# Kernel optimization log

Hardware: AMD Instinct MI355X
Metric: run time of the kernel (lower is better)

## Reference

```python
import math
import jax, jax.numpy as jnp
import numpy as np

N, E = 4096, 131072
IN_DIM, HID_DIM, OUT_DIM = 1024, 512, 128
PE_IN, PE_HID, K = 128, 64, 10
PE_ALPHA, PE_BETA = 0.1, 0.5


def _glorot(k, shape):
    fan = shape[0] + shape[-1]
    return jax.random.normal(k, shape, dtype=jnp.float32) * (2.0 / fan) ** 0.5


def setup_inputs() -> dict:
    key = jax.random.key(0)
    ks = jax.random.split(key, 12)
    return {
        "node_feat": jax.random.normal(ks[0], (N, IN_DIM), dtype=jnp.float32),
        "edge_index": jax.random.randint(ks[1], (2, E), 0, N, dtype=jnp.int64),
        "pos_enc": jax.random.normal(ks[2], (N, PE_IN), dtype=jnp.float32),
        "lin1_w": _glorot(ks[3], (IN_DIM, HID_DIM)),
        "lin1_b": jnp.zeros((HID_DIM,), jnp.float32),
        "lin2_w": _glorot(ks[4], (HID_DIM, OUT_DIM)),
        "lin2_b": jnp.zeros((OUT_DIM,), jnp.float32),
        "pe_w": _glorot(ks[5], (PE_IN, PE_HID)),
        "pe_b": jnp.zeros((PE_HID,), jnp.float32),
        "cor_w": _glorot(ks[6], (PE_HID, PE_HID)),
        "cor_b": jnp.zeros((PE_HID,), jnp.float32),
        "gate_w": _glorot(ks[7], (K + 1, PE_HID)),
        "gate_b": jnp.zeros((K + 1,), jnp.float32),
        "temp": jnp.ones((K + 1,), jnp.float32),
    }


def reference(node_feat, edge_index, pos_enc, lin1_w, lin1_b, lin2_w, lin2_b,
              pe_w, pe_b, cor_w, cor_b, gate_w, gate_b, temp):
    n = node_feat.shape[0]
    src, dst = edge_index[0], edge_index[1]
    ew = jnp.ones(src.shape[0], dtype=node_feat.dtype)

    # sym-normalized adjacency A_norm = D^-1/2 A D^-1/2 (deg on source row, per PyG get_laplacian)
    deg = jax.ops.segment_sum(ew, src, num_segments=n)
    dinv = jnp.where(deg > 0, deg ** -0.5, 0.0)
    wl = dinv[src] * dinv[dst]

    def anorm(x):  # scatter-add message passing: out[i] = sum_j w_ij x[j]
        return jax.ops.segment_sum(wl[:, None] * x[src], dst, num_segments=n)

    # gcn_norm with self-loops: Ahat = Dhat^-1/2 (A + I) Dhat^-1/2 (deg on target col)
    deg2 = jax.ops.segment_sum(ew, dst, num_segments=n) + 1.0
    d2 = deg2 ** -0.5
    wg = d2[src] * d2[dst]

    def ahat(p):
        return jax.ops.segment_sum(wg[:, None] * p[src], dst, num_segments=n) + (d2 * d2)[:, None] * p

    # encoders
    pe = jnp.tanh(pos_enc @ pe_w + pe_b)
    x = jax.nn.relu(node_feat @ lin1_w + lin1_b) @ lin2_w + lin2_b

    TEMP = jax.nn.relu(temp)
    # tmp[k] = (2I - L)^k x, and (2I - L)x = x + A_norm x
    tmp = [x]
    for _ in range(K):
        x = x + anorm(x)
        tmp.append(x)

    coeff = [math.comb(K, i) / 2 ** K for i in range(K + 1)]
    gamma0 = TEMP[0] * jax.nn.sigmoid((pe @ gate_w[0])[:, None] + gate_b[0])  # [N,1]
    out = coeff[0] * gamma0 * tmp[K]

    raw_pe = pe
    for i in range(K):
        xi = tmp[K - i - 1]
        for _ in range(i + 1):  # apply L = I - A_norm, (i+1) times
            xi = xi - anorm(xi)
        # PE correlation propagation: dense NxN sigmoid adjacency
        c = pe @ cor_w + cor_b
        pe_corr = jax.nn.sigmoid(c @ c.T) @ pe
        pe_tpo = ahat(pe)
        pe = (1.0 + PE_BETA) * pe_tpo - PE_BETA * pe_corr
        pe = PE_ALPHA * raw_pe + (1.0 - PE_ALPHA) * pe
        pe = jnp.tanh(pe)
        gamma = TEMP[i + 1] * jax.nn.sigmoid((pe @ gate_w[i + 1])[:, None] + gate_b[i + 1])
        out = out + coeff[i + 1] * gamma * xi
    return (out, pe)
```

## Files before the change

### kernel.cpp

```cpp
#include <hip/hip_runtime.h>
#include <math.h>

constexpr int N_NODES = 4096;
constexpr int E_EDGES = 131072;
constexpr int IND     = 1024;
constexpr int HID     = 512;
constexpr int OUTD    = 128;
constexpr int PEH     = 64;
constexpr int KHOP    = 10;
constexpr int NPE     = N_NODES * PEH;
constexpr int NM      = N_NODES * OUTD;
constexpr int NCHUNK  = 16;

__constant__ float d_coeff[11] = {
    1.f/1024.f, 10.f/1024.f, 45.f/1024.f, 120.f/1024.f, 210.f/1024.f,
    252.f/1024.f, 210.f/1024.f, 120.f/1024.f, 45.f/1024.f, 10.f/1024.f, 1.f/1024.f};

__constant__ float d_beta[11][11] = {
    {1,  10, 45, 120, 210, 252, 210, 120, 45, 10, 1},
    {1,   8, 27,  48,  42,   0, -42, -48, -27, -8, -1},
    {1,   6, 13,   8, -14, -28, -14,   8,  13,  6,  1},
    {1,   4,  3,  -8, -14,   0,  14,   8,  -3, -4, -1},
    {1,   2, -3,  -8,   2,  12,   2,  -8,  -3,  2,  1},
    {1,   0, -5,   0,  10,   0, -10,   0,   5,  0, -1},
    {1,  -2, -3,   8,   2, -12,   2,   8,  -3, -2,  1},
    {1,  -4,  3,   8, -14,   0,  14,  -8,  -3,  4, -1},
    {1,  -6, 13,  -8, -14,  28, -14,  -8,  13, -6,  1},
    {1,  -8, 27, -48,  42,   0, -42,  48, -27,  8, -1},
    {1, -10, 45, -120, 210, -252, 210, -120, 45, -10, 1}};

typedef __attribute__((ext_vector_type(8))) short bf16x8;
typedef __attribute__((ext_vector_type(4))) float f32x4;

__device__ __forceinline__ void split_bf16(float x, short& h, short& l) {
    unsigned bx = __float_as_uint(x);
    h = (short)(bx >> 16);
    float hf = __uint_as_float(bx & 0xffff0000u);
    l = (short)(__float_as_uint(x - hf) >> 16);
}

__device__ __forceinline__ size_t fidx(int g, int T, int t, int h, int lane) {
    return ((((size_t)g * T + t) * 2 + h) * 64 + lane) * 8;
}

__device__ __forceinline__ int swz(int row, int col) {
    return row * 64 + (col ^ ((row & 7) << 3));
}

__global__ void k_degrees(const int* __restrict__ src, const int* __restrict__ dst,
                          int* outdeg, int* indeg) {
    int e = blockIdx.x * blockDim.x + threadIdx.x;
    if (e < E_EDGES) {
        atomicAdd(&outdeg[src[e]], 1);
        atomicAdd(&indeg[dst[e]], 1);
    }
}

__global__ void k_invs(const int* __restrict__ outdeg, const int* __restrict__ indeg,
                       float* dinv, float* d2) {
    int i = blockIdx.x * blockDim.x + threadIdx.x;
    if (i < N_NODES) {
        int od = outdeg[i];
        dinv[i] = od > 0 ? 1.0f / sqrtf((float)od) : 0.0f;
        d2[i]   = 1.0f / sqrtf((float)indeg[i] + 1.0f);
    }
}

__global__ void k_scan(const int* __restrict__ cnt, int* __restrict__ rp) {
    int lane = threadIdx.x;
    int base = lane * 64;
    int sum = 0;
    for (int j = 0; j < 64; ++j) sum += cnt[base + j];
    int incl = sum;
    for (int off = 1; off < 64; off <<= 1) {
        int nv = __shfl_up(incl, off);
        if (lane >= off) incl += nv;
    }
    int run = incl - sum;
    for (int j = 0; j < 64; ++j) { rp[base + j] = run; run += cnt[base + j]; }
    if (lane == 63) rp[N_NODES] = run;
}

__global__ void k_scatter(const int* __restrict__ src, const int* __restrict__ dst,
                          const int* __restrict__ rp, int* __restrict__ fill,
                          const float* __restrict__ dinv, const float* __restrict__ d2,
                          int* __restrict__ col, float* __restrict__ wl,
                          float* __restrict__ wg) {
    int e = blockIdx.x * blockDim.x + threadIdx.x;
    if (e < E_EDGES) {
        int s = src[e], d = dst[e];
        int pos = rp[d] + atomicAdd(&fill[d], 1);
        col[pos] = s;
        wl[pos]  = dinv[s] * dinv[d];
        wg[pos]  = d2[s] * d2[d];
    }
}

__global__ void k_split_rm(const float* __restrict__ in, ushort* __restrict__ oh,
                           ushort* __restrict__ ol, int total8) {
    int i = blockIdx.x * blockDim.x + threadIdx.x;
    if (i >= total8) return;
    int r = i >> 7, c8 = i & 127;
    float4 f0 = *(const float4*)&in[(size_t)i * 8];
    float4 f1 = *(const float4*)&in[(size_t)i * 8 + 4];
    float v[8] = {f0.x, f0.y, f0.z, f0.w, f1.x, f1.y, f1.z, f1.w};
    bf16x8 h, l;
#pragma unroll
    for (int j = 0; j < 8; ++j) {
        short hh, ll;
        split_bf16(v[j], hh, ll);
        h[j] = hh; l[j] = ll;
    }
    int t = c8 >> 3, hh2 = (c8 >> 2) & 1, lq = c8 & 3;
    size_t a = fidx(r >> 4, IND / 64, t, hh2, lq * 16 + (r & 15));
    *(bf16x8*)&oh[a] = h;
    *(bf16x8*)&ol[a] = l;
}

__global__ __launch_bounds__(256) void k_splitT(const float* __restrict__ in,
                                                ushort* __restrict__ th,
                                                ushort* __restrict__ tl,
                                                int R, int C) {
    __shared__ float tile[64][65];
    int tid = threadIdx.x;
    int r0 = blockIdx.x * 64, c0 = blockIdx.y * 64;
    int row = tid >> 2, cq = (tid & 3) * 16;
#pragma unroll
    for (int q = 0; q < 4; ++q) {
        float4 f = *(const float4*)&in[(size_t)(r0 + row) * C + c0 + cq + q * 4];
        tile[row][cq + q * 4 + 0] = f.x;
        tile[row][cq + q * 4 + 1] = f.y;
        tile[row][cq + q * 4 + 2] = f.z;
        tile[row][cq + q * 4 + 3] = f.w;
    }
    __syncthreads();
    int d = tid & 63, q = tid >> 6;
    bf16x8 h0, h1, l0, l1;
#pragma unroll
    for (int c = 0; c < 8; ++c) {
        short hh, ll;
        split_bf16(tile[q * 16 + c][d], hh, ll);
        h0[c] = hh; l0[c] = ll;
    }
#pragma unroll
    for (int c = 0; c < 8; ++c) {
        short hh, ll;
        split_bf16(tile[q * 16 + 8 + c][d], hh, ll);
        h1[c] = hh; l1[c] = ll;
    }
    int T = R / 64;
    int g = (c0 + d) >> 4, lm = (c0 + d) & 15, t = r0 >> 6, hh2 = q >> 1;
    size_t a0 = fidx(g, T, t, hh2, ((2 * q) & 3) * 16 + lm);
    size_t a1 = fidx(g, T, t, hh2, ((2 * q + 1) & 3) * 16 + lm);
    *(bf16x8*)&th[a0] = h0;
    *(bf16x8*)&th[a1] = h1;
    *(bf16x8*)&tl[a0] = l0;
    *(bf16x8*)&tl[a1] = l1;
}

template <int T, int KCH>
__global__ __launch_bounds__(256) void k_xgemm_zp(const ushort* __restrict__ apkh,
                                                  const ushort* __restrict__ apkl,
                                                  const ushort* __restrict__ bpkh,
                                                  const ushort* __restrict__ bpkl,
                                                  float* __restrict__ pout) {
    int tid = threadIdx.x;
    int w = tid >> 6, l = tid & 63;
    int ga = blockIdx.x * 4 + w;
    int gb0 = blockIdx.y * 4;
    int t0 = blockIdx.z * (KCH / 64);
    f32x4 acc[4];
#pragma unroll
    for (int n = 0; n < 4; ++n) acc[n] = (f32x4){0.f, 0.f, 0.f, 0.f};
    for (int kk = 0; kk < KCH / 64; ++kk) {
        int t = t0 + kk;
        bf16x8 Ah0 = *(const bf16x8*)&apkh[fidx(ga, T, t, 0, l)];
        bf16x8 Ah1 = *(const bf16x8*)&apkh[fidx(ga, T, t, 1, l)];
        bf16x8 Al0 = *(const bf16x8*)&apkl[fidx(ga, T, t, 0, l)];
        bf16x8 Al1 = *(const bf16x8*)&apkl[fidx(ga, T, t, 1, l)];
#pragma unroll
        for (int n = 0; n < 4; ++n) {
            bf16x8 Bh0 = *(const bf16x8*)&bpkh[fidx(gb0 + n, T, t, 0, l)];
            bf16x8 Bh1 = *(const bf16x8*)&bpkh[fidx(gb0 + n, T, t, 1, l)];
            bf16x8 Bl0 = *(const bf16x8*)&bpkl[fidx(gb0 + n, T, t, 0, l)];
            bf16x8 Bl1 = *(const bf16x8*)&bpkl[fidx(gb0 + n, T, t, 1, l)];
            acc[n] = __builtin_amdgcn_mfma_f32_16x16x32_bf16(Ah0, Bh0, acc[n], 0, 0, 0);
            acc[n] = __builtin_amdgcn_mfma_f32_16x16x32_bf16(Ah1, Bh1, acc[n], 0, 0, 0);
            acc[n] = __builtin_amdgcn_mfma_f32_16x16x32_bf16(Ah0, Bl0, acc[n], 0, 0, 0);
            acc[n] = __builtin_amdgcn_mfma_f32_16x16x32_bf16(Ah1, Bl1, acc[n], 0, 0, 0);
            acc[n] = __builtin_amdgcn_mfma_f32_16x16x32_bf16(Al0, Bh0, acc[n], 0, 0, 0);
            acc[n] = __builtin_amdgcn_mfma_f32_16x16x32_bf16(Al1, Bh1, acc[n], 0, 0, 0);
        }
    }
    size_t base = ((((size_t)blockIdx.z * gridDim.x + blockIdx.x) * gridDim.y)
                   + blockIdx.y) * 4096;
#pragma unroll
    for (int n = 0; n < 4; ++n) {
#pragma unroll
        for (int r = 0; r < 4; ++r) {
            pout[base + (size_t)(w * 16 + n * 4 + r) * 64 + l] = acc[n][r];
        }
    }
}

template <int NC, bool RELU, bool SPLIT>
__global__ void k_finzp(const float* __restrict__ pin, const float* __restrict__ bias,
                        float* __restrict__ outf, ushort* __restrict__ oh,
                        ushort* __restrict__ ol) {
    constexpr int GY = NC / 64;
    constexpr size_t ZSTEP = (size_t)64 * GY * 4096;
    int i8 = blockIdx.x * blockDim.x + threadIdx.x;
    int r = i8 / (NC / 8), c = (i8 % (NC / 8)) * 8;
    int bx = r >> 6, w = (r >> 4) & 3, lq = (r >> 2) & 3, rr = r & 3;
    int by = c >> 6, n = (c >> 4) & 3, lm0 = c & 15;
    size_t base = (((size_t)bx * GY) + by) * 4096
                  + (size_t)(w * 16 + n * 4 + rr) * 64 + lq * 16 + lm0;
    float v[8];
#pragma unroll
    for (int j = 0; j < 8; ++j) v[j] = bias[c + j];
#pragma unroll
    for (int z = 0; z < 4; ++z) {
        float4 p0 = *(const float4*)&pin[base + z * ZSTEP];
        float4 p1 = *(const float4*)&pin[base + z * ZSTEP + 4];
        v[0] += p0.x; v[1] += p0.y; v[2] += p0.z; v[3] += p0.w;
        v[4] += p1.x; v[5] += p1.y; v[6] += p1.z; v[7] += p1.w;
    }
    if (RELU) {
#pragma unroll
        for (int j = 0; j < 8; ++j) v[j] = fmaxf(v[j], 0.f);
    }
    if (SPLIT) {
        bf16x8 h, lo;
#pragma unroll
        for (int j = 0; j < 8; ++j) {
            short hh, ll;
            split_bf16(v[j], hh, ll);
            h[j] = hh; lo[j] = ll;
        }
        size_t a = fidx(r >> 4, NC / 64, c >> 6, (c >> 5) & 1,
                        ((c >> 3) & 3) * 16 + (r & 15));
        *(bf16x8*)&oh[a] = h;
        *(bf16x8*)&ol[a] = lo;
    } else {
        *(float4*)&outf[(size_t)r * NC + c] =
            make_float4(v[0], v[1], v[2], v[3]);
        *(float4*)&outf[(size_t)r * NC + c + 4] =
            make_float4(v[4], v[5], v[6], v[7]);
    }
}

__global__ __launch_bounds__(256) void k_pe0(const float* __restrict__ pos_enc,
                                             const float* __restrict__ pw,
                                             const float* __restrict__ pb,
                                             float* __restrict__ pe,
                                             float* __restrict__ raw,
                                             ushort* __restrict__ pthpk,
                                             ushort* __restrict__ ptlpk,
                                             const float* __restrict__ gw,
                                             const float* __restrict__ gb,
                                             const float* __restrict__ temp,
                                             float* __restrict__ gamma) {
    __shared__ float tile[64][65];
    int tid = threadIdx.x, w = tid >> 6, l = tid & 63;
    int nloc = w * 16 + (l >> 2);
    int nn = blockIdx.x * 64 + nloc;
    int f0 = (l & 3) * 16;
    float v[16];
#pragma unroll
    for (int f = 0; f < 16; ++f) v[f] = pb[f0 + f];
    for (int k0 = 0; k0 < 128; k0 += 4) {
        float4 pv = *(const float4*)&pos_enc[(size_t)nn * 128 + k0];
        float pa[4] = {pv.x, pv.y, pv.z, pv.w};
#pragma unroll
        for (int kk = 0; kk < 4; ++kk) {
            const float* wr = &pw[(size_t)(k0 + kk) * 64 + f0];
            float4 w0 = *(const float4*)&wr[0];
            float4 w1 = *(const float4*)&wr[4];
            float4 w2 = *(const float4*)&wr[8];
            float4 w3 = *(const float4*)&wr[12];
            float wv[16] = {w0.x, w0.y, w0.z, w0.w, w1.x, w1.y, w1.z, w1.w,
                            w2.x, w2.y, w2.z, w2.w, w3.x, w3.y, w3.z, w3.w};
#pragma unroll
            for (int f = 0; f < 16; ++f) v[f] = fmaf(pa[kk], wv[f], v[f]);
        }
    }
#pragma unroll
    for (int f = 0; f < 16; ++f) v[f] = tanhf(v[f]);
#pragma unroll
    for (int q = 0; q < 4; ++q) {
        float4 fv = make_float4(v[q * 4], v[q * 4 + 1], v[q * 4 + 2], v[q * 4 + 3]);
        *(float4*)&pe[(size_t)nn * 64 + f0 + q * 4] = fv;
        *(float4*)&raw[(size_t)nn * 64 + f0 + q * 4] = fv;
    }
    float g = 0.f;
#pragma unroll
    for (int f = 0; f < 16; ++f) g = fmaf(v[f], gw[f0 + f], g);
    g += __shfl_xor(g, 1);
    g += __shfl_xor(g, 2);
    if ((l & 3) == 0) {
        float T = temp[0];
        T = T > 0.f ? T : 0.f;
        gamma[nn] = T / (1.f + expf(-(g + gb[0])));
    }
#pragma unroll
    for (int f = 0; f < 16; ++f) tile[nloc][f0 + f] = v[f];
    __syncthreads();
    int d = l, q = w;
    bf16x8 h0, h1, l0, l1;
#pragma unroll
    for (int c = 0; c < 8; ++c) {
        short hh, ll;
        split_bf16(tile[q * 16 + c][d], hh, ll);
        h0[c] = hh; l0[c] = ll;
    }
#pragma unroll
    for (int c = 0; c < 8; ++c) {
        short hh, ll;
        split_bf16(tile[q * 16 + 8 + c][d], hh, ll);
        h1[c] = hh; l1[c] = ll;
    }
    int ng = d >> 4, lm = d & 15, tcb = blockIdx.x, hh2 = q >> 1;
    size_t a0 = fidx(ng, 64, tcb, hh2, ((2 * q) & 3) * 16 + lm);
    size_t a1 = fidx(ng, 64, tcb, hh2, ((2 * q + 1) & 3) * 16 + lm);
    *(bf16x8*)&pthpk[a0] = h0;
    *(bf16x8*)&pthpk[a1] = h1;
    *(bf16x8*)&ptlpk[a0] = l0;
    *(bf16x8*)&ptlpk[a1] = l1;
}

__global__ void k_cmat(const float* __restrict__ pe, const float* __restrict__ cw,
                       const float* __restrict__ cb, ushort* __restrict__ chpk,
                       ushort* __restrict__ clpk) {
    int t = threadIdx.x;
    int r = blockIdx.x * 4 + threadIdx.y;
    float acc = cb[t];
    for (int k = 0; k < PEH; ++k)
        acc = fmaf(pe[(size_t)r * PEH + k], cw[k * PEH + t], acc);
    short hh, ll;
    split_bf16(acc, hh, ll);
    size_t a = fidx(r >> 4, 1, 0, t >> 5, ((t >> 3) & 3) * 16 + (r & 15)) + (t & 7);
    chpk[a] = (ushort)hh;
    clpk[a] = (ushort)ll;
}

__global__ __launch_bounds__(256) void k_corr5(const ushort* __restrict__ chpk,
                                               const ushort* __restrict__ clpk,
                                               const ushort* __restrict__ pthpk,
                                               const ushort* __restrict__ ptlpk,
                                               float* __restrict__ part) {
    __shared__ __align__(16) ushort Sh[4096];
    __shared__ __align__(16) ushort Sl[4096];
    int tid = threadIdx.x, w = tid >> 6, l = tid & 63;
    int lm = l & 15, lq = l >> 4, wrow = w * 16;
    int chunk = blockIdx.y;

    int ga = blockIdx.x * 4 + w;
    bf16x8 cAh0 = *(const bf16x8*)&chpk[fidx(ga, 1, 0, 0, l)];
    bf16x8 cAh1 = *(const bf16x8*)&chpk[fidx(ga, 1, 0, 1, l)];
    bf16x8 cAl0 = *(const bf16x8*)&clpk[fidx(ga, 1, 0, 0, l)];
    bf16x8 cAl1 = *(const bf16x8*)&clpk[fidx(ga, 1, 0, 1, l)];

    f32x4 pacc[4];
#pragma unroll
    for (int n = 0; n < 4; ++n) pacc[n] = (f32x4){0.f, 0.f, 0.f, 0.f};

#pragma unroll
    for (int tt = 0; tt < 4; ++tt) {
#pragma unroll
        for (int n = 0; n < 4; ++n) {
            int gb = chunk * 16 + tt * 4 + n;
            bf16x8 Bh0 = *(const bf16x8*)&chpk[fidx(gb, 1, 0, 0, l)];
            bf16x8 Bh1 = *(const bf16x8*)&chpk[fidx(gb, 1, 0, 1, l)];
            bf16x8 Bl0 = *(const bf16x8*)&clpk[fidx(gb, 1, 0, 0, l)];
            bf16x8 Bl1 = *(const bf16x8*)&clpk[fidx(gb, 1, 0, 1, l)];
            f32x4 sacc = (f32x4){0.f, 0.f, 0.f, 0.f};
            sacc = __builtin_amdgcn_mfma_f32_16x16x32_bf16(cAh0, Bh0, sacc, 0, 0, 0);
            sacc = __builtin_amdgcn_mfma_f32_16x16x32_bf16(cAh1, Bh1, sacc, 0, 0, 0);
            sacc = __builtin_amdgcn_mfma_f32_16x16x32_bf16(cAh0, Bl0, sacc, 0, 0, 0);
            sacc = __builtin_amdgcn_mfma_f32_16x16x32_bf16(cAh1, Bl1, sacc, 0, 0, 0);
            sacc = __builtin_amdgcn_mfma_f32_16x16x32_bf16(cAl0, Bh0, sacc, 0, 0, 0);
            sacc = __builtin_amdgcn_mfma_f32_16x16x32_bf16(cAl1, Bh1, sacc, 0, 0, 0);
#pragma unroll
            for (int r = 0; r < 4; ++r) {
                float sg = 1.0f / (1.0f + __expf(-sacc[r]));
                short hh, ll;
                split_bf16(sg, hh, ll);
                int iw = swz(wrow + lq * 4 + r, n * 16 + lm);
                Sh[iw] = (ushort)hh;
                Sl[iw] = (ushort)ll;
            }
        }
        bf16x8 sAh0 = *(const bf16x8*)&Sh[swz(wrow + lm, lq * 8)];
        bf16x8 sAh1 = *(const bf16x8*)&Sh[swz(wrow + lm, 32 + lq * 8)];
        bf16x8 sAl0 = *(const bf16x8*)&Sl[swz(wrow + lm, lq * 8)];
        bf16x8 sAl1 = *(const bf16x8*)&Sl[swz(wrow + lm, 32 + lq * 8)];
        int tc = chunk * 4 + tt;
#pragma unroll
        for (int n = 0; n < 4; ++n) {
            bf16x8 Ph0 = *(const bf16x8*)&pthpk[fidx(n, 64, tc, 0, l)];
            bf16x8 Ph1 = *(const bf16x8*)&pthpk[fidx(n, 64, tc, 1, l)];
            bf16x8 Pl0 = *(const bf16x8*)&ptlpk[fidx(n, 64, tc, 0, l)];
            bf16x8 Pl1 = *(const bf16x8*)&ptlpk[fidx(n, 64, tc, 1, l)];
            pacc[n] = __builtin_amdgcn_mfma_f32_16x16x32_bf16(sAh0, Ph0, pacc[n], 0, 0, 0);
            pacc[n] = __builtin_amdgcn_mfma_f32_16x16x32_bf16(sAh1, Ph1, pacc[n], 0, 0, 0);
            pacc[n] = __builtin_amdgcn_mfma_f32_16x16x32_bf16(sAh0, Pl0, pacc[n], 0, 0, 0);
            pacc[n] = __builtin_amdgcn_mfma_f32_16x16x32_bf16(sAh1, Pl1, pacc[n], 0, 0, 0);
            pacc[n] = __builtin_amdgcn_mfma_f32_16x16x32_bf16(sAl0, Ph0, pacc[n], 0, 0, 0);
            pacc[n] = __builtin_amdgcn_mfma_f32_16x16x32_bf16(sAl1, Ph1, pacc[n], 0, 0, 0);
        }
    }
    size_t base = ((size_t)chunk * 64 + blockIdx.x) * 4096;
#pragma unroll
    for (int n = 0; n < 4; ++n) {
#pragma unroll
        for (int r = 0; r < 4; ++r) {
            part[base + (size_t)(w * 16 + n * 4 + r) * 64 + l] = pacc[n][r];
        }
    }
}

__global__ void k_csum(const float* __restrict__ corrp, float* __restrict__ corrsum) {
    int i8 = blockIdx.x * blockDim.x + threadIdx.x;
    int half = blockIdx.y;
    int r = i8 >> 3, d = (i8 & 7) * 8;
    int bx = r >> 6, w = (r >> 4) & 3, lq = (r >> 2) & 3, rr = r & 3;
    int n = (d >> 4) & 3, lm0 = d & 15;
    size_t inblk = (size_t)(w * 16 + n * 4 + rr) * 64 + lq * 16 + lm0;
    float v[8] = {0.f, 0.f, 0.f, 0.f, 0.f, 0.f, 0.f, 0.f};
#pragma unroll
    for (int p = 0; p < 8; ++p) {
        int chunk = half * 8 + p;
        const float* s = &corrp[((size_t)chunk * 64 + bx) * 4096 + inblk];
        float4 p0 = *(const float4*)&s[0];
        float4 p1 = *(const float4*)&s[4];
        v[0] += p0.x; v[1] += p0.y; v[2] += p0.z; v[3] += p0.w;
        v[4] += p1.x; v[5] += p1.y; v[6] += p1.z; v[7] += p1.w;
    }
    float* o = &corrsum[(size_t)half * NPE + (size_t)r * 64 + d];
    *(float4*)&o[0] = make_float4(v[0], v[1], v[2], v[3]);
    *(float4*)&o[4] = make_float4(v[4], v[5], v[6], v[7]);
}

__global__ void k_ahat(const float* __restrict__ pe, float* __restrict__ tpo,
                       const int* __restrict__ rp, const int* __restrict__ col,
                       const float* __restrict__ wg, const float* __restrict__ d2) {
    __shared__ int sc[64];
    __shared__ float sw[64];
    int r = blockIdx.x, t = threadIdx.x;
    int e0 = rp[r], e1 = rp[r + 1];
    float dd = d2[r];
    float acc = dd * dd * pe[(size_t)r * PEH + t];
    for (int ch = e0; ch < e1; ch += 64) {
        int n = min(64, e1 - ch);
        __syncthreads();
        if (t < n) { sc[t] = col[ch + t]; sw[t] = wg[ch + t]; }
        __syncthreads();
        for (int q = 0; q < n; ++q)
            acc = fmaf(sw[q], pe[(size_t)sc[q] * PEH + t], acc);
    }
    tpo[(size_t)r * PEH + t] = acc;
}

__global__ __launch_bounds__(256) void k_update(const float* __restrict__ tpo,
                                                const float* __restrict__ corrsum,
                                                const float* __restrict__ raw,
                                                float* __restrict__ pe,
                                                const float* __restrict__ gw,
                                                const float* __restrict__ gb,
                                                const float* __restrict__ temp,
                                                float* __restrict__ gamma,
                                                ushort* __restrict__ pthpk,
                                                ushort* __restrict__ ptlpk, int ip1) {
    __shared__ float tile[64][65];
    int tid = threadIdx.x, w = tid >> 6, l = tid & 63;
    int nloc = w * 16 + (l >> 2);
    int nn = blockIdx.x * 64 + nloc;
    int f0 = (l & 3) * 16;
    size_t idx = (size_t)nn * 64 + f0;
    float v[16];
#pragma unroll
    for (int q = 0; q < 4; ++q) {
        float4 tp = *(const float4*)&tpo[idx + q * 4];
        float4 rw = *(const float4*)&raw[idx + q * 4];
        float4 c0 = *(const float4*)&corrsum[idx + q * 4];
        float4 c1 = *(const float4*)&corrsum[(size_t)NPE + idx + q * 4];
        float tv[4] = {tp.x, tp.y, tp.z, tp.w};
        float rv[4] = {rw.x, rw.y, rw.z, rw.w};
        float cr[4] = {c0.x + c1.x, c0.y + c1.y, c0.z + c1.z, c0.w + c1.w};
#pragma unroll
        for (int e = 0; e < 4; ++e) {
            float x = 1.5f * tv[e] - 0.5f * cr[e];
            x = 0.1f * rv[e] + 0.9f * x;
            v[q * 4 + e] = tanhf(x);
        }
    }
#pragma unroll
    for (int q = 0; q < 4; ++q) {
        *(float4*)&pe[idx + q * 4] =
            make_float4(v[q * 4], v[q * 4 + 1], v[q * 4 + 2], v[q * 4 + 3]);
    }
    float g = 0.f;
#pragma unroll
    for (int f = 0; f < 16; ++f) g = fmaf(v[f], gw[ip1 * PEH + f0 + f], g);
    g += __shfl_xor(g, 1);
    g += __shfl_xor(g, 2);
    if ((l & 3) == 0) {
        float T = temp[ip1];
        T = T > 0.f ? T : 0.f;
        gamma[ip1 * N_NODES + nn] = T / (1.f + expf(-(g + gb[ip1])));
    }
#pragma unroll
    for (int f = 0; f < 16; ++f) tile[nloc][f0 + f] = v[f];
    __syncthreads();
    int d = l, q = w;
    bf16x8 h0, h1, l0, l1;
#pragma unroll
    for (int c = 0; c < 8; ++c) {
        short hh, ll;
        split_bf16(tile[q * 16 + c][d], hh, ll);
        h0[c] = hh; l0[c] = ll;
    }
#pragma unroll
    for (int c = 0; c < 8; ++c) {
        short hh, ll;
        split_bf16(tile[q * 16 + 8 + c][d], hh, ll);
        h1[c] = hh; l1[c] = ll;
    }
    int ng = d >> 4, lm = d & 15, tcb = blockIdx.x, hh2 = q >> 1;
    size_t a0 = fidx(ng, 64, tcb, hh2, ((2 * q) & 3) * 16 + lm);
    size_t a1 = fidx(ng, 64, tcb, hh2, ((2 * q + 1) & 3) * 16 + lm);
    *(bf16x8*)&pthpk[a0] = h0;
    *(bf16x8*)&pthpk[a1] = h1;
    *(bf16x8*)&ptlpk[a0] = l0;
    *(bf16x8*)&ptlpk[a1] = l1;
}

__global__ void k_spmm(const float* __restrict__ in, float* __restrict__ outp,
                       const int* __restrict__ rp, const int* __restrict__ col,
                       const float* __restrict__ w) {
    __shared__ int sc[128];
    __shared__ float sw[128];
    int r = blockIdx.x, t = threadIdx.x;
    int e0 = rp[r], e1 = rp[r + 1];
    float acc = 0.f;
    for (int ch = e0; ch < e1; ch += 128) {
        int n = min(128, e1 - ch);
        __syncthreads();
        if (t < n) { sc[t] = col[ch + t]; sw[t] = w[ch + t]; }
        __syncthreads();
        for (int q = 0; q < n; ++q)
            acc = fmaf(sw[q], in[(size_t)sc[q] * OUTD + t], acc);
    }
    outp[(size_t)r * OUTD + t] = acc;
}

__global__ void k_out(const float* __restrict__ y, const float* __restrict__ gamma,
                      float* __restrict__ dout) {
    int r = blockIdx.x, t = threadIdx.x;
    float g[11];
#pragma unroll
    for (int j = 0; j <= KHOP; ++j) g[j] = d_coeff[j] * gamma[j * N_NODES + r];
    float acc = 0.f;
#pragma unroll
    for (int m = 0; m <= KHOP; ++m) {
        float dm = 0.f;
#pragma unroll
        for (int j = 0; j <= KHOP; ++j) dm = fmaf(g[j], d_beta[j][m], dm);
        acc = fmaf(dm, y[(size_t)m * NM + (size_t)r * OUTD + t], acc);
    }
    dout[(size_t)r * OUTD + t] = acc;
}

__global__ void k_pecopy(const float* __restrict__ pe, float* __restrict__ dout) {
    int i = blockIdx.x * blockDim.x + threadIdx.x;
    if (i < NPE) dout[NM + i] = pe[i];
}

extern "C" void kernel_launch(void* const* d_in, const int* in_sizes, int n_in,
                              void* d_out, int out_size, void* d_ws, size_t ws_size,
                              hipStream_t stream) {
    const float* node_feat = (const float*)d_in[0];
    const int*   eidx      = (const int*)d_in[1];
    const float* pos_enc   = (const float*)d_in[2];
    const float* lin1_w    = (const float*)d_in[3];
    const float* lin1_b    = (const float*)d_in[4];
    const float* lin2_w    = (const float*)d_in[5];
    const float* lin2_b    = (const float*)d_in[6];
    const float* pe_w      = (const float*)d_in[7];
    const float* pe_b      = (const float*)d_in[8];
    const float* cor_w     = (const float*)d_in[9];
    const float* cor_b     = (const float*)d_in[10];
    const float* gate_w    = (const float*)d_in[11];
    const float* gate_b    = (const float*)d_in[12];
    const float* temp      = (const float*)d_in[13];
    const int* src = eidx;
    const int* dst = eidx + E_EDGES;
    float* dout = (float*)d_out;

    char* p = (char*)d_ws;
    auto alloc = [&](size_t bytes) -> char* {
        char* r = p;
        p += (bytes + 255) & ~(size_t)255;
        return r;
    };
    int*    outdeg = (int*)alloc(N_NODES * 4);
    int*    indeg  = (int*)alloc(N_NODES * 4);
    int*    fill   = (int*)alloc(N_NODES * 4);
    int*    rp     = (int*)alloc((N_NODES + 1) * 4);
    int*    col    = (int*)alloc(E_EDGES * 4);
    float*  wl     = (float*)alloc(E_EDGES * 4);
    float*  wg     = (float*)alloc(E_EDGES * 4);
    float*  dinv   = (float*)alloc(N_NODES * 4);
    float*  d2     = (float*)alloc(N_NODES * 4);
    ushort* nfh    = (ushort*)alloc((size_t)N_NODES * IND * 2);
    ushort* nfl    = (ushort*)alloc((size_t)N_NODES * IND * 2);
    ushort* w1th   = (ushort*)alloc((size_t)HID * IND * 2);
    ushort* w1tl   = (ushort*)alloc((size_t)HID * IND * 2);
    ushort* w2th   = (ushort*)alloc((size_t)OUTD * HID * 2);
    ushort* w2tl   = (ushort*)alloc((size_t)OUTD * HID * 2);
    ushort* hh     = (ushort*)alloc((size_t)N_NODES * HID * 2);
    ushort* hl     = (ushort*)alloc((size_t)N_NODES * HID * 2);
    float*  pe     = (float*)alloc((size_t)NPE * 4);
    float*  raw    = (float*)alloc((size_t)NPE * 4);
    ushort* pth    = (ushort*)alloc((size_t)NPE * 2);
    ushort* ptl    = (ushort*)alloc((size_t)NPE * 2);
    ushort* ch     = (ushort*)alloc((size_t)NPE * 2);
    ushort* cl     = (ushort*)alloc((size_t)NPE * 2);
    float*  tpo    = (float*)alloc((size_t)NPE * 4);
    float*  pacc1  = (float*)alloc((size_t)4 * N_NODES * HID * 4);
    float*  corrp  = pacc1;
    float*  pacc2  = (float*)alloc((size_t)4 * N_NODES * OUTD * 4);
    float*  corrsum= pacc2;
    float*  gamma  = (float*)alloc((size_t)11 * N_NODES * 4);
    float*  y      = (float*)alloc((size_t)11 * NM * 4);

    hipMemsetAsync(outdeg, 0, N_NODES * 4, stream);
    hipMemsetAsync(indeg, 0, N_NODES * 4, stream);
    hipMemsetAsync(fill, 0, N_NODES * 4, stream);

    k_degrees<<<E_EDGES / 256, 256, 0, stream>>>(src, dst, outdeg, indeg);
    k_invs<<<N_NODES / 256, 256, 0, stream>>>(outdeg, indeg, dinv, d2);
    k_scan<<<1, 64, 0, stream>>>(indeg, rp);
    k_scatter<<<E_EDGES / 256, 256, 0, stream>>>(src, dst, rp, fill, dinv, d2, col, wl, wg);

    k_split_rm<<<(N_NODES * IND / 8 + 255) / 256, 256, 0, stream>>>(
        node_feat, nfh, nfl, N_NODES * IND / 8);
    k_splitT<<<dim3(IND / 64, HID / 64), 256, 0, stream>>>(lin1_w, w1th, w1tl, IND, HID);
    k_splitT<<<dim3(HID / 64, OUTD / 64), 256, 0, stream>>>(lin2_w, w2th, w2tl, HID, OUTD);

    k_xgemm_zp<16, 256><<<dim3(64, 8, 4), 256, 0, stream>>>(nfh, nfl, w1th, w1tl, pacc1);
    k_finzp<HID, true, true><<<(N_NODES * HID / 8) / 256, 256, 0, stream>>>(
        pacc1, lin1_b, nullptr, hh, hl);
    k_xgemm_zp<8, 128><<<dim3(64, 2, 4), 256, 0, stream>>>(hh, hl, w2th, w2tl, pacc2);
    k_finzp<OUTD, false, false><<<(N_NODES * OUTD / 8) / 256, 256, 0, stream>>>(
        pacc2, lin2_b, y, nullptr, nullptr);

    k_pe0<<<N_NODES / 64, 256, 0, stream>>>(pos_enc, pe_w, pe_b, pe, raw, pth, ptl,
                                            gate_w, gate_b, temp, gamma);

    for (int m = 1; m <= KHOP; ++m) {
        k_spmm<<<N_NODES, 128, 0, stream>>>(y + (size_t)(m - 1) * NM,
                                            y + (size_t)m * NM, rp, col, wl);
    }

    for (int i = 0; i < KHOP; ++i) {
        k_cmat<<<N_NODES / 4, dim3(64, 4), 0, stream>>>(pe, cor_w, cor_b, ch, cl);
        k_corr5<<<dim3(N_NODES / 64, NCHUNK), 256, 0, stream>>>(ch, cl, pth, ptl, corrp);
        k_csum<<<dim3(NPE / 8 / 256, 2), 256, 0, stream>>>(corrp, corrsum);
        k_ahat<<<N_NODES, 64, 0, stream>>>(pe, tpo, rp, col, wg, d2);
        k_update<<<N_NODES / 64, 256, 0, stream>>>(tpo, corrsum, raw, pe, gate_w,
                                                   gate_b, temp, gamma, pth, ptl, i + 1);
    }

    k_out<<<N_NODES, 128, 0, stream>>>(y, gamma, dout);
    k_pecopy<<<(NPE + 255) / 256, 256, 0, stream>>>(pe, dout);
}
```

Measured before the change: 766.3 us.

## Fuse PE iteration kernels and prefetch B operands in correlation GEMM

Fuses the per-iteration c = pe@cor_w computation into the update kernel, and folds the partial-sum reduction of the correlation chunks into the ahat SpMM kernel. It also writes the final pe straight into the output, which drops the copy kernel. The correlation kernel now loads its packed PE operands before the LDS reads so memory latency overlaps the MFMA work, and k_pe0 is retiled to 16 nodes per block for more parallelism. Together these cut about two launches per iteration plus some global round trips, at the cost of heavier fused kernels and more register pressure.

```diff
diff --git a/kernel.cpp b/kernel.cpp
--- a/kernel.cpp
+++ b/kernel.cpp
@@ -260,72 +260,65 @@
                                              const float* __restrict__ gb,
                                              const float* __restrict__ temp,
                                              float* __restrict__ gamma) {
-    __shared__ float tile[64][65];
-    int tid = threadIdx.x, w = tid >> 6, l = tid & 63;
-    int nloc = w * 16 + (l >> 2);
-    int nn = blockIdx.x * 64 + nloc;
-    int f0 = (l & 3) * 16;
-    float v[16];
-#pragma unroll
-    for (int f = 0; f < 16; ++f) v[f] = pb[f0 + f];
+    __shared__ float tile[16][65];
+    int tid = threadIdx.x, s = tid >> 6, d = tid & 63;
+    int n0 = blockIdx.x * 16;
+    int nb = n0 + s * 4;
+    float bv = pb[d];
+    float v[4] = {bv, bv, bv, bv};
     for (int k0 = 0; k0 < 128; k0 += 4) {
-        float4 pv = *(const float4*)&pos_enc[(size_t)nn * 128 + k0];
-        float pa[4] = {pv.x, pv.y, pv.z, pv.w};
+        float4 p0 = *(const float4*)&pos_enc[(size_t)(nb + 0) * 128 + k0];
+        float4 p1 = *(const float4*)&pos_enc[(size_t)(nb + 1) * 128 + k0];
+        float4 p2 = *(const float4*)&pos_enc[(size_t)(nb + 2) * 128 + k0];
+        float4 p3 = *(const float4*)&pos_enc[(size_t)(nb + 3) * 128 + k0];
+        float pa0[4] = {p0.x, p0.y, p0.z, p0.w};
+        float pa1[4] = {p1.x, p1.y, p1.z, p1.w};
+        float pa2[4] = {p2.x, p2.y, p2.z, p2.w};
+        float pa3[4] = {p3.x, p3.y, p3.z, p3.w};
 #pragma unroll
         for (int kk = 0; kk < 4; ++kk) {
-            const float* wr = &pw[(size_t)(k0 + kk) * 64 + f0];
-            float4 w0 = *(const float4*)&wr[0];
-            float4 w1 = *(const float4*)&wr[4];
-            float4 w2 = *(const float4*)&wr[8];
-            float4 w3 = *(const float4*)&wr[12];
-            float wv[16] = {w0.x, w0.y, w0.z, w0.w, w1.x, w1.y, w1.z, w1.w,
-                            w2.x, w2.y, w2.z, w2.w, w3.x, w3.y, w3.z, w3.w};
-#pragma unroll
-            for (int f = 0; f < 16; ++f) v[f] = fmaf(pa[kk], wv[f], v[f]);
-        }
-    }
-#pragma unroll
-    for (int f = 0; f < 16; ++f) v[f] = tanhf(v[f]);
-#pragma unroll
-    for (int q = 0; q < 4; ++q) {
-        float4 fv = make_float4(v[q * 4], v[q * 4 + 1], v[q * 4 + 2], v[q * 4 + 3]);
-        *(float4*)&pe[(size_t)nn * 64 + f0 + q * 4] = fv;
-        *(float4*)&raw[(size_t)nn * 64 + f0 + q * 4] = fv;
-    }
-    float g = 0.f;
-#pragma unroll
-    for (int f = 0; f < 16; ++f) g = fmaf(v[f], gw[f0 + f], g);
-    g += __shfl_xor(g, 1);
-    g += __shfl_xor(g, 2);
-    if ((l & 3) == 0) {
-        float T = temp[0];
-        T = T > 0.f ? T : 0.f;
-        gamma[nn] = T / (1.f + expf(-(g + gb[0])));
-    }
-#pragma unroll
-    for (int f = 0; f < 16; ++f) tile[nloc][f0 + f] = v[f];
+            float wv = pw[(size_t)(k0 + kk) * 64 + d];
+            v[0] = fmaf(pa0[kk], wv, v[0]);
+            v[1] = fmaf(pa1[kk], wv, v[1]);
+            v[2] = fmaf(pa2[kk], wv, v[2]);
+            v[3] = fmaf(pa3[kk], wv, v[3]);
+        }
+    }
+#pragma unroll
+    for (int j = 0; j < 4; ++j) v[j] = tanhf(v[j]);
+#pragma unroll
+    for (int j = 0; j < 4; ++j) {
+        pe[(size_t)(nb + j) * 64 + d]  = v[j];
+        raw[(size_t)(nb + j) * 64 + d] = v[j];
+        tile[s * 4 + j][d] = v[j];
+    }
+    float gwv = gw[d];
+#pragma unroll
+    for (int j = 0; j < 4; ++j) {
+        float g = v[j] * gwv;
+        for (int m = 32; m; m >>= 1) g += __shfl_xor(g, m);
+        if (d == 0) {
+            float T = temp[0];
+            T = T > 0.f ? T : 0.f;
+            gamma[nb + j] = T / (1.f + expf(-(g + gb[0])));
+        }
+    }
     __syncthreads();
-    int d = l, q = w;
-    bf16x8 h0, h1, l0, l1;
-#pragma unroll
-    for (int c = 0; c < 8; ++c) {
-        short hh, ll;
-        split_bf16(tile[q * 16 + c][d], hh, ll);
-        h0[c] = hh; l0[c] = ll;
-    }
-#pragma unroll
-    for (int c = 0; c < 8; ++c) {
-        short hh, ll;
-        split_bf16(tile[q * 16 + 8 + c][d], hh, ll);
-        h1[c] = hh; l1[c] = ll;
-    }
-    int ng = d >> 4, lm = d & 15, tcb = blockIdx.x, hh2 = q >> 1;
-    size_t a0 = fidx(ng, 64, tcb, hh2, ((2 * q) & 3) * 16 + lm);
-    size_t a1 = fidx(ng, 64, tcb, hh2, ((2 * q + 1) & 3) * 16 + lm);
-    *(bf16x8*)&pthpk[a0] = h0;
-    *(bf16x8*)&pthpk[a1] = h1;
-    *(bf16x8*)&ptlpk[a0] = l0;
-    *(bf16x8*)&ptlpk[a1] = l1;
+    if (tid < 128) {
+        int o = tid >> 6, dd = tid & 63;
+        bf16x8 h, lo;
+#pragma unroll
+        for (int e = 0; e < 8; ++e) {
+            short hh, ll;
+            split_bf16(tile[o * 8 + e][dd], hh, ll);
+            h[e] = hh; lo[e] = ll;
+        }
+        int off = (n0 & 63) + o * 8;
+        int h2 = off >> 5, lq3 = (off >> 3) & 3;
+        size_t a = fidx(dd >> 4, 64, n0 >> 6, h2, lq3 * 16 + (dd & 15));
+        *(bf16x8*)&pthpk[a] = h;
+        *(bf16x8*)&ptlpk[a] = lo;
+    }
 }
 
 __global__ void k_cmat(const float* __restrict__ pe, const float* __restrict__ cw,
@@ -343,7 +336,7 @@
     clpk[a] = (ushort)ll;
 }
 
-__global__ __launch_bounds__(256) void k_corr5(const ushort* __restrict__ chpk,
+__global__ __launch_bounds__(256) void k_corr6(const ushort* __restrict__ chpk,
                                                const ushort* __restrict__ clpk,
                                                const ushort* __restrict__ pthpk,
                                                const ushort* __restrict__ ptlpk,
@@ -390,23 +383,27 @@
                 Sl[iw] = (ushort)ll;
             }
         }
+        int tc = chunk * 4 + tt;
+        bf16x8 Ph0[4], Ph1[4], Pl0[4], Pl1[4];
+#pragma unroll
+        for (int n = 0; n < 4; ++n) {
+            Ph0[n] = *(const bf16x8*)&pthpk[fidx(n, 64, tc, 0, l)];
+            Ph1[n] = *(const bf16x8*)&pthpk[fidx(n, 64, tc, 1, l)];
+            Pl0[n] = *(const bf16x8*)&ptlpk[fidx(n, 64, tc, 0, l)];
+            Pl1[n] = *(const bf16x8*)&ptlpk[fidx(n, 64, tc, 1, l)];
+        }
         bf16x8 sAh0 = *(const bf16x8*)&Sh[swz(wrow + lm, lq * 8)];
         bf16x8 sAh1 = *(const bf16x8*)&Sh[swz(wrow + lm, 32 + lq * 8)];
         bf16x8 sAl0 = *(const bf16x8*)&Sl[swz(wrow + lm, lq * 8)];
         bf16x8 sAl1 = *(const bf16x8*)&Sl[swz(wrow + lm, 32 + lq * 8)];
-        int tc = chunk * 4 + tt;
 #pragma unroll
         for (int n = 0; n < 4; ++n) {
-            bf16x8 Ph0 = *(const bf16x8*)&pthpk[fidx(n, 64, tc, 0, l)];
-            bf16x8 Ph1 = *(const bf16x8*)&pthpk[fidx(n, 64, tc, 1, l)];
-            bf16x8 Pl0 = *(const bf16x8*)&ptlpk[fidx(n, 64, tc, 0, l)];
-            bf16x8 Pl1 = *(const bf16x8*)&ptlpk[fidx(n, 64, tc, 1, l)];
-            pacc[n] = __builtin_amdgcn_mfma_f32_16x16x32_bf16(sAh0, Ph0, pacc[n], 0, 0, 0);
-            pacc[n] = __builtin_amdgcn_mfma_f32_16x16x32_bf16(sAh1, Ph1, pacc[n], 0, 0, 0);
-            pacc[n] = __builtin_amdgcn_mfma_f32_16x16x32_bf16(sAh0, Pl0, pacc[n], 0, 0, 0);
-            pacc[n] = __builtin_amdgcn_mfma_f32_16x16x32_bf16(sAh1, Pl1, pacc[n], 0, 0, 0);
-            pacc[n] = __builtin_amdgcn_mfma_f32_16x16x32_bf16(sAl0, Ph0, pacc[n], 0, 0, 0);
-            pacc[n] = __builtin_amdgcn_mfma_f32_16x16x32_bf16(sAl1, Ph1, pacc[n], 0, 0, 0);
+            pacc[n] = __builtin_amdgcn_mfma_f32_16x16x32_bf16(sAh0, Ph0[n], pacc[n], 0, 0, 0);
+            pacc[n] = __builtin_amdgcn_mfma_f32_16x16x32_bf16(sAh1, Ph1[n], pacc[n], 0, 0, 0);
+            pacc[n] = __builtin_amdgcn_mfma_f32_16x16x32_bf16(sAh0, Pl0[n], pacc[n], 0, 0, 0);
+            pacc[n] = __builtin_amdgcn_mfma_f32_16x16x32_bf16(sAh1, Pl1[n], pacc[n], 0, 0, 0);
+            pacc[n] = __builtin_amdgcn_mfma_f32_16x16x32_bf16(sAl0, Ph0[n], pacc[n], 0, 0, 0);
+            pacc[n] = __builtin_amdgcn_mfma_f32_16x16x32_bf16(sAl1, Ph1[n], pacc[n], 0, 0, 0);
         }
     }
     size_t base = ((size_t)chunk * 64 + blockIdx.x) * 4096;
@@ -419,34 +416,23 @@
     }
 }
 
-__global__ void k_csum(const float* __restrict__ corrp, float* __restrict__ corrsum) {
-    int i8 = blockIdx.x * blockDim.x + threadIdx.x;
-    int half = blockIdx.y;
-    int r = i8 >> 3, d = (i8 & 7) * 8;
-    int bx = r >> 6, w = (r >> 4) & 3, lq = (r >> 2) & 3, rr = r & 3;
-    int n = (d >> 4) & 3, lm0 = d & 15;
-    size_t inblk = (size_t)(w * 16 + n * 4 + rr) * 64 + lq * 16 + lm0;
-    float v[8] = {0.f, 0.f, 0.f, 0.f, 0.f, 0.f, 0.f, 0.f};
-#pragma unroll
-    for (int p = 0; p < 8; ++p) {
-        int chunk = half * 8 + p;
-        const float* s = &corrp[((size_t)chunk * 64 + bx) * 4096 + inblk];
-        float4 p0 = *(const float4*)&s[0];
-        float4 p1 = *(const float4*)&s[4];
-        v[0] += p0.x; v[1] += p0.y; v[2] += p0.z; v[3] += p0.w;
-        v[4] += p1.x; v[5] += p1.y; v[6] += p1.z; v[7] += p1.w;
-    }
-    float* o = &corrsum[(size_t)half * NPE + (size_t)r * 64 + d];
-    *(float4*)&o[0] = make_float4(v[0], v[1], v[2], v[3]);
-    *(float4*)&o[4] = make_float4(v[4], v[5], v[6], v[7]);
-}
-
-__global__ void k_ahat(const float* __restrict__ pe, float* __restrict__ tpo,
-                       const int* __restrict__ rp, const int* __restrict__ col,
-                       const float* __restrict__ wg, const float* __restrict__ d2) {
+__global__ void k_ahat_cs(const float* __restrict__ pe, float* __restrict__ tpo,
+                          const int* __restrict__ rp, const int* __restrict__ col,
+                          const float* __restrict__ wg, const float* __restrict__ d2,
+                          const float* __restrict__ corrp,
+                          float* __restrict__ corrsum) {
     __shared__ int sc[64];
     __shared__ float sw[64];
     int r = blockIdx.x, t = threadIdx.x;
+    {
+        int bx = r >> 6, w = (r >> 4) & 3, lq = (r >> 2) & 3, rr = r & 3;
+        size_t inblk = (size_t)(w * 16 + (t >> 4) * 4 + rr) * 64 + lq * 16 + (t & 15);
+        float s = 0.f;
+#pragma unroll
+        for (int p = 0; p < NCHUNK; ++p)
+            s += corrp[((size_t)p * 64 + bx) * 4096 + inblk];
+        corrsum[(size_t)r * PEH + t] = s;
+    }
     int e0 = rp[r], e1 = rp[r + 1];
     float dd = d2[r];
     float acc = dd * dd * pe[(size_t)r * PEH + t];
@@ -461,16 +447,21 @@
     tpo[(size_t)r * PEH + t] = acc;
 }
 
-__global__ __launch_bounds__(256) void k_update(const float* __restrict__ tpo,
-                                                const float* __restrict__ corrsum,
-                                                const float* __restrict__ raw,
-                                                float* __restrict__ pe,
-                                                const float* __restrict__ gw,
-                                                const float* __restrict__ gb,
-                                                const float* __restrict__ temp,
-                                                float* __restrict__ gamma,
-                                                ushort* __restrict__ pthpk,
-                                                ushort* __restrict__ ptlpk, int ip1) {
+__global__ __launch_bounds__(256) void k_update2(const float* __restrict__ tpo,
+                                                 const float* __restrict__ corrsum,
+                                                 const float* __restrict__ raw,
+                                                 float* __restrict__ pe,
+                                                 const float* __restrict__ gw,
+                                                 const float* __restrict__ gb,
+                                                 const float* __restrict__ temp,
+                                                 float* __restrict__ gamma,
+                                                 ushort* __restrict__ pthpk,
+                                                 ushort* __restrict__ ptlpk,
+                                                 const float* __restrict__ cw,
+                                                 const float* __restrict__ cb,
+                                                 ushort* __restrict__ chpk,
+                                                 ushort* __restrict__ clpk,
+                                                 float* __restrict__ peout, int ip1) {
     __shared__ float tile[64][65];
     int tid = threadIdx.x, w = tid >> 6, l = tid & 63;
     int nloc = w * 16 + (l >> 2);
@@ -483,10 +474,9 @@
         float4 tp = *(const float4*)&tpo[idx + q * 4];
         float4 rw = *(const float4*)&raw[idx + q * 4];
         float4 c0 = *(const float4*)&corrsum[idx + q * 4];
-        float4 c1 = *(const float4*)&corrsum[(size_t)NPE + idx + q * 4];
         float tv[4] = {tp.x, tp.y, tp.z, tp.w};
         float rv[4] = {rw.x, rw.y, rw.z, rw.w};
-        float cr[4] = {c0.x + c1.x, c0.y + c1.y, c0.z + c1.z, c0.w + c1.w};
+        float cr[4] = {c0.x, c0.y, c0.z, c0.w};
 #pragma unroll
         for (int e = 0; e < 4; ++e) {
             float x = 1.5f * tv[e] - 0.5f * cr[e];
@@ -496,8 +486,9 @@
     }
 #pragma unroll
     for (int q = 0; q < 4; ++q) {
-        *(float4*)&pe[idx + q * 4] =
-            make_float4(v[q * 4], v[q * 4 + 1], v[q * 4 + 2], v[q * 4 + 3]);
+        float4 fv = make_float4(v[q * 4], v[q * 4 + 1], v[q * 4 + 2], v[q * 4 + 3]);
+        *(float4*)&pe[idx + q * 4] = fv;
+        if (peout) *(float4*)&peout[idx + q * 4] = fv;
     }
     float g = 0.f;
 #pragma unroll
@@ -512,27 +503,63 @@
 #pragma unroll
     for (int f = 0; f < 16; ++f) tile[nloc][f0 + f] = v[f];
     __syncthreads();
-    int d = l, q = w;
-    bf16x8 h0, h1, l0, l1;
-#pragma unroll
-    for (int c = 0; c < 8; ++c) {
-        short hh, ll;
-        split_bf16(tile[q * 16 + c][d], hh, ll);
-        h0[c] = hh; l0[c] = ll;
-    }
-#pragma unroll
-    for (int c = 0; c < 8; ++c) {
-        short hh, ll;
-        split_bf16(tile[q * 16 + 8 + c][d], hh, ll);
-        h1[c] = hh; l1[c] = ll;
-    }
-    int ng = d >> 4, lm = d & 15, tcb = blockIdx.x, hh2 = q >> 1;
-    size_t a0 = fidx(ng, 64, tcb, hh2, ((2 * q) & 3) * 16 + lm);
-    size_t a1 = fidx(ng, 64, tcb, hh2, ((2 * q + 1) & 3) * 16 + lm);
-    *(bf16x8*)&pthpk[a0] = h0;
-    *(bf16x8*)&pthpk[a1] = h1;
-    *(bf16x8*)&ptlpk[a0] = l0;
-    *(bf16x8*)&ptlpk[a1] = l1;
+    {
+        int d = l, q = w;
+        bf16x8 h0, h1, l0, l1;
+#pragma unroll
+        for (int c = 0; c < 8; ++c) {
+            short hh, ll;
+            split_bf16(tile[q * 16 + c][d], hh, ll);
+            h0[c] = hh; l0[c] = ll;
+        }
+#pragma unroll
+        for (int c = 0; c < 8; ++c) {
+            short hh, ll;
+            split_bf16(tile[q * 16 + 8 + c][d], hh, ll);
+            h1[c] = hh; l1[c] = ll;
+        }
+        int ng = d >> 4, lm = d & 15, tcb = blockIdx.x, hh2 = q >> 1;
+        size_t a0 = fidx(ng, 64, tcb, hh2, ((2 * q) & 3) * 16 + lm);
+        size_t a1 = fidx(ng, 64, tcb, hh2, ((2 * q + 1) & 3) * 16 + lm);
+        *(bf16x8*)&pthpk[a0] = h0;
+        *(bf16x8*)&pthpk[a1] = h1;
+        *(bf16x8*)&ptlpk[a0] = l0;
+        *(bf16x8*)&ptlpk[a1] = l1;
+    }
+    {
+        int node = tid >> 2;
+        int d0 = (tid & 3) * 16;
+        float c16[16];
+#pragma unroll
+        for (int j = 0; j < 16; ++j) c16[j] = cb[d0 + j];
+        for (int k = 0; k < 64; ++k) {
+            float pv = tile[node][k];
+            const float* wr = &cw[(size_t)k * 64 + d0];
+            float4 w0 = *(const float4*)&wr[0];
+            float4 w1 = *(const float4*)&wr[4];
+            float4 w2 = *(const float4*)&wr[8];
+            float4 w3 = *(const float4*)&wr[12];
+            float wv[16] = {w0.x, w0.y, w0.z, w0.w, w1.x, w1.y, w1.z, w1.w,
+                            w2.x, w2.y, w2.z, w2.w, w3.x, w3.y, w3.z, w3.w};
+#pragma unroll
+            for (int j = 0; j < 16; ++j) c16[j] = fmaf(pv, wv[j], c16[j]);
+        }
+        int r = blockIdx.x * 64 + node;
+#pragma unroll
+        for (int hf = 0; hf < 2; ++hf) {
+            int d = d0 + hf * 8;
+            bf16x8 h, lo;
+#pragma unroll
+            for (int e = 0; e < 8; ++e) {
+                short hh, ll;
+                split_bf16(c16[hf * 8 + e], hh, ll);
+                h[e] = hh; lo[e] = ll;
+            }
+            size_t a = fidx(r >> 4, 1, 0, d >> 5, ((d >> 3) & 3) * 16 + (r & 15));
+            *(bf16x8*)&chpk[a] = h;
+            *(bf16x8*)&clpk[a] = lo;
+        }
+    }
 }
 
 __global__ void k_spmm(const float* __restrict__ in, float* __restrict__ outp,
@@ -569,11 +596,6 @@
         acc = fmaf(dm, y[(size_t)m * NM + (size_t)r * OUTD + t], acc);
     }
     dout[(size_t)r * OUTD + t] = acc;
-}
-
-__global__ void k_pecopy(const float* __restrict__ pe, float* __restrict__ dout) {
-    int i = blockIdx.x * blockDim.x + threadIdx.x;
-    if (i < NPE) dout[NM + i] = pe[i];
 }
 
 extern "C" void kernel_launch(void* const* d_in, const int* in_sizes, int n_in,
@@ -655,7 +677,7 @@
     k_finzp<OUTD, false, false><<<(N_NODES * OUTD / 8) / 256, 256, 0, stream>>>(
         pacc2, lin2_b, y, nullptr, nullptr);
 
-    k_pe0<<<N_NODES / 64, 256, 0, stream>>>(pos_enc, pe_w, pe_b, pe, raw, pth, ptl,
+    k_pe0<<<N_NODES / 16, 256, 0, stream>>>(pos_enc, pe_w, pe_b, pe, raw, pth, ptl,
                                             gate_w, gate_b, temp, gamma);
 
     for (int m = 1; m <= KHOP; ++m) {
@@ -663,15 +685,16 @@
                                             y + (size_t)m * NM, rp, col, wl);
     }
 
+    k_cmat<<<N_NODES / 4, dim3(64, 4), 0, stream>>>(pe, cor_w, cor_b, ch, cl);
+
     for (int i = 0; i < KHOP; ++i) {
-        k_cmat<<<N_NODES / 4, dim3(64, 4), 0, stream>>>(pe, cor_w, cor_b, ch, cl);
-        k_corr5<<<dim3(N_NODES / 64, NCHUNK), 256, 0, stream>>>(ch, cl, pth, ptl, corrp);
-        k_csum<<<dim3(NPE / 8 / 256, 2), 256, 0, stream>>>(corrp, corrsum);
-        k_ahat<<<N_NODES, 64, 0, stream>>>(pe, tpo, rp, col, wg, d2);
-        k_update<<<N_NODES / 64, 256, 0, stream>>>(tpo, corrsum, raw, pe, gate_w,
-                                                   gate_b, temp, gamma, pth, ptl, i + 1);
+        k_corr6<<<dim3(N_NODES / 64, NCHUNK), 256, 0, stream>>>(ch, cl, pth, ptl, corrp);
+        k_ahat_cs<<<N_NODES, 64, 0, stream>>>(pe, tpo, rp, col, wg, d2, corrp, corrsum);
+        float* peout = (i == KHOP - 1) ? (dout + NM) : nullptr;
+        k_update2<<<N_NODES / 64, 256, 0, stream>>>(tpo, corrsum, raw, pe, gate_w,
+                                                    gate_b, temp, gamma, pth, ptl,
+                                                    cor_w, cor_b, ch, cl, peout, i + 1);
     }
 
     k_out<<<N_NODES, 128, 0, stream>>>(y, gamma, dout);
-    k_pecopy<<<(NPE + 255) / 256, 256, 0, stream>>>(pe, dout);
-}
+}
```

After: 875.0 us. +14.2%, slower.
